# Kernel tuning notes

Hardware: AMD Instinct MI355X
Metric: run time of the kernel (lower is better)

The kernel has to match this reference:

```python
import jax, jax.numpy as jnp
import numpy as np

T, H = 2048, 2048            # tokens, hidden_size
NQ, NKV, D = 32, 4, 128      # q heads, kv heads, head_dim
E, K, I, CAP = 64, 8, 768, 512  # experts, top_k, moe_intermediate, per-expert capacity
EPS, THETA = 1e-6, 10000.0


def setup_inputs() -> dict:
    key = jax.random.key(0)
    ks = jax.random.split(key, 10)
    n = lambda k, shp, sc: jax.random.normal(k, shp, jnp.float32) * sc
    return {
        "hidden_states": n(ks[0], (T, H), 1.0),
        "positions": jnp.arange(T, dtype=jnp.int32),
        "wqkv": n(ks[1], (H, (NQ + 2 * NKV) * D), H ** -0.5),
        "wo": n(ks[2], (NQ * D, H), (NQ * D) ** -0.5),
        "q_norm_w": jnp.ones((D,), jnp.float32),
        "k_norm_w": jnp.ones((D,), jnp.float32),
        "ln1_w": jnp.ones((H,), jnp.float32),
        "ln2_w": jnp.ones((H,), jnp.float32),
        "gate_w": n(ks[3], (H, E), H ** -0.5),
        "w_gate": n(ks[4], (E, H, I), H ** -0.5),
        "w_up": n(ks[5], (E, H, I), H ** -0.5),
        "w_down": n(ks[6], (E, I, H), I ** -0.5),
    }


def _rmsnorm(x, w):
    v = jnp.mean(jnp.square(x.astype(jnp.float32)), axis=-1, keepdims=True)
    return (x.astype(jnp.float32) * jax.lax.rsqrt(v + EPS)).astype(x.dtype) * w


def _rope(x, cos, sin):
    # x: [T, heads, D]; neox-style rotate-half over full head_dim
    x1, x2 = x[..., : D // 2], x[..., D // 2:]
    c, s = cos[:, None, :], sin[:, None, :]
    return jnp.concatenate([x1 * c - x2 * s, x2 * c + x1 * s], axis=-1)


def _forward(hidden_states, positions, wqkv, wo, q_norm_w, k_norm_w, ln1_w, ln2_w, gate_w, w_gate, w_up, w_down):
    x = hidden_states
    # ---- input RMSNorm + GQA attention with QK-norm + RoPE ----
    h = _rmsnorm(x, ln1_w)
    qkv = h @ wqkv
    q, k, v = jnp.split(qkv, [NQ * D, NQ * D + NKV * D], axis=-1)
    q = _rmsnorm(q.reshape(T, NQ, D), q_norm_w)
    k = _rmsnorm(k.reshape(T, NKV, D), k_norm_w)
    v = v.reshape(T, NKV, D)
    inv_freq = 1.0 / (THETA ** (jnp.arange(0, D, 2, dtype=jnp.float32) / D))
    ang = positions.astype(jnp.float32)[:, None] * inv_freq  # [T, D/2]
    cos, sin = jnp.cos(ang), jnp.sin(ang)
    q, k = _rope(q, cos, sin), _rope(k, cos, sin)
    rep = NQ // NKV
    kr = jnp.repeat(k, rep, axis=1)  # [T, NQ, D]
    vr = jnp.repeat(v, rep, axis=1)
    scores = jnp.einsum('qhd,khd->hqk', q, kr) * (D ** -0.5)
    causal = jnp.tril(jnp.ones((T, T), bool))
    scores = jnp.where(causal[None], scores, -1e30)
    probs = jax.nn.softmax(scores, axis=-1)
    attn = jnp.einsum('hqk,khd->qhd', probs, vr).reshape(T, NQ * D)
    x = x + attn @ wo
    # ---- post-attn RMSNorm + sparse MoE (softmax top-k routing, renormalized) ----
    h = _rmsnorm(x, ln2_w)
    logits = h @ gate_w
    gate_probs = jax.nn.softmax(logits.astype(jnp.float32), axis=-1)
    topk_w, topk_idx = jax.lax.top_k(gate_probs, K)              # [T, K]
    topk_w = topk_w / jnp.sum(topk_w, axis=-1, keepdims=True)    # norm_topk_prob
    flat_e = topk_idx.reshape(-1)                                # [T*K], row-major
    oh = jax.nn.one_hot(flat_e, E, dtype=jnp.int32)
    pos = jnp.sum(jnp.cumsum(oh, axis=0) * oh, axis=-1) - 1      # slot within expert
    x_rep = jnp.repeat(h, K, axis=0)                             # [T*K, H]
    buf = jnp.zeros((E, CAP, H), h.dtype).at[flat_e, pos].set(x_rep, mode='drop')
    g = jnp.einsum('ech,ehi->eci', buf, w_gate)
    u = jnp.einsum('ech,ehi->eci', buf, w_up)
    act = jax.nn.silu(g) * u
    out_buf = jnp.einsum('eci,eih->ech', act, w_down)
    valid = (pos < CAP).astype(h.dtype)                          # CAP >> expected load; no drops in practice
    gathered = out_buf[flat_e, jnp.clip(pos, 0, CAP - 1)]        # [T*K, H]
    w = topk_w.reshape(-1).astype(h.dtype) * valid
    moe_out = jnp.sum((gathered * w[:, None]).reshape(T, K, H), axis=1)
    return x + moe_out


def reference(hidden_states, positions, wqkv, wo, q_norm_w, k_norm_w, ln1_w, ln2_w, gate_w, w_gate, w_up, w_down):
    return _forward(hidden_states, positions, wqkv, wo, q_norm_w, k_norm_w,
                    ln1_w, ln2_w, gate_w, w_gate, w_up, w_down)
```

## Files before the change

kernel.cpp:

```cpp
#include <hip/hip_runtime.h>
#include <hip/hip_bf16.h>

#define T_    2048
#define H_    2048
#define NQ_   32
#define NKV_  4
#define D_    128
#define E_    64
#define TK_   8
#define I_    768
#define CAP_  512
#define QKVW_ 5120

typedef float  f32x4  __attribute__((ext_vector_type(4)));
typedef __bf16 bf16x8 __attribute__((ext_vector_type(8)));
typedef int    i32x4  __attribute__((ext_vector_type(4)));
#define AS1 __attribute__((address_space(1)))
#define AS3 __attribute__((address_space(3)))

static __device__ __forceinline__ unsigned f2bf_u(float f){
  unsigned u = __builtin_bit_cast(unsigned, f);
  u += 0x7fffu + ((u >> 16) & 1u);
  return u >> 16;
}
static __device__ __forceinline__ float bf2f(unsigned h){
  unsigned u = h << 16;
  return __builtin_bit_cast(float, u);
}
struct HL { int h; int l; };
static __device__ __forceinline__ HL packsplit(float a, float b){
  unsigned ah = f2bf_u(a), bh = f2bf_u(b);
  float al = a - bf2f(ah), bl = b - bf2f(bh);
  HL r;
  r.h = (int)(ah | (bh << 16));
  r.l = (int)(f2bf_u(al) | (f2bf_u(bl) << 16));
  return r;
}
static __device__ __forceinline__ f32x4 mfma16(bf16x8 a, bf16x8 b, f32x4 c){
  return __builtin_amdgcn_mfma_f32_16x16x32_bf16(a, b, c, 0, 0, 0);
}

__global__ __launch_bounds__(256) void k_rms(const float* __restrict__ in,
                                             const float* __restrict__ w,
                                             unsigned short* __restrict__ outh,
                                             unsigned short* __restrict__ outl,
                                             float* __restrict__ cpy)
{
  const int t = blockIdx.x, tid = threadIdx.x;
  const float* row = in + (long)t * H_;
  float4 a = *(const float4*)(row + tid*8);
  float4 b = *(const float4*)(row + tid*8 + 4);
  float ss = a.x*a.x + a.y*a.y + a.z*a.z + a.w*a.w
           + b.x*b.x + b.y*b.y + b.z*b.z + b.w*b.w;
  #pragma unroll
  for (int o = 32; o >= 1; o >>= 1) ss += __shfl_xor(ss, o);
  __shared__ float red[4];
  if ((tid & 63) == 0) red[tid >> 6] = ss;
  __syncthreads();
  float tot = red[0] + red[1] + red[2] + red[3];
  float rs = rsqrtf(tot * (1.0f / (float)H_) + 1e-6f);
  const float* wp = w + tid*8;
  float vv[8] = {a.x, a.y, a.z, a.w, b.x, b.y, b.z, b.w};
  i32x4 oh, ol;
  #pragma unroll
  for (int d = 0; d < 4; d++){
    float v0 = vv[2*d]   * rs * wp[2*d];
    float v1 = vv[2*d+1] * rs * wp[2*d+1];
    HL r = packsplit(v0, v1);
    oh[d] = r.h; ol[d] = r.l;
  }
  *(i32x4*)(outh + (long)t * H_ + tid*8) = oh;
  if (outl) *(i32x4*)(outl + (long)t * H_ + tid*8) = ol;
  if (cpy){
    *(float4*)(cpy + (long)t * H_ + tid*8)     = a;
    *(float4*)(cpy + (long)t * H_ + tid*8 + 4) = b;
  }
}

__global__ __launch_bounds__(64) void k_ropetab(const int* __restrict__ pos,
                                                float* __restrict__ cosb,
                                                float* __restrict__ sinb)
{
  int t = blockIdx.x, j = threadIdx.x;
  float p = (float)pos[t];
  float freq = expf(-(float)j * (2.0f / (float)D_) * 9.210340371976184f);
  float ang = p * freq;
  cosb[t*64 + j] = cosf(ang);
  sinb[t*64 + j] = sinf(ang);
}

__global__ __launch_bounds__(256) void k_qknorm(const float* __restrict__ qkv,
                                                const float* __restrict__ qw,
                                                const float* __restrict__ kw,
                                                const float* __restrict__ cosb,
                                                const float* __restrict__ sinb,
                                                unsigned short* __restrict__ qh,
                                                unsigned short* __restrict__ ql,
                                                unsigned short* __restrict__ khp,
                                                unsigned short* __restrict__ klp)
{
  int gw = blockIdx.x*4 + (threadIdx.x >> 6);
  int lane = threadIdx.x & 63;
  int t = gw / 36, hh = gw - t*36;
  const float* src; const float* w;
  unsigned short *dh, *dl;
  if (hh < NQ_){
    src = qkv + (long)t*QKVW_ + hh*D_;
    w = qw;
    dh = qh + ((long)t*NQ_ + hh)*D_;
    dl = ql + ((long)t*NQ_ + hh)*D_;
  } else {
    int kh = hh - NQ_;
    src = qkv + (long)t*QKVW_ + NQ_*D_ + kh*D_;
    w = kw;
    dh = khp + ((long)t*NKV_ + kh)*D_;
    dl = klp + ((long)t*NKV_ + kh)*D_;
  }
  float a = src[lane], b = src[lane + 64];
  float ss = a*a + b*b;
  #pragma unroll
  for (int o = 32; o >= 1; o >>= 1) ss += __shfl_xor(ss, o);
  float rs = rsqrtf(ss * (1.0f / (float)D_) + 1e-6f);
  a *= rs * w[lane];
  b *= rs * w[lane + 64];
  float c = cosb[t*64 + lane], s = sinb[t*64 + lane];
  float r0 = a*c - b*s;
  float r1 = b*c + a*s;
  unsigned h0 = f2bf_u(r0), h1 = f2bf_u(r1);
  dh[lane]      = (unsigned short)h0;
  dh[lane + 64] = (unsigned short)h1;
  dl[lane]      = (unsigned short)f2bf_u(r0 - bf2f(h0));
  dl[lane + 64] = (unsigned short)f2bf_u(r1 - bf2f(h1));
}

__global__ __launch_bounds__(256) void k_vtrans(const float* __restrict__ qkv,
                                                unsigned short* __restrict__ vth,
                                                unsigned short* __restrict__ vtl)
{
  __shared__ unsigned short tileh[64][136];
  __shared__ unsigned short tilel[64][136];
  const int t0 = blockIdx.x * 64;
  const int hv = blockIdx.y;
  const int tid = threadIdx.x;
  #pragma unroll
  for (int it = 0; it < 8; it++){
    int chunk = tid + it*256;
    int r  = chunk >> 5;
    int c4 = chunk & 31;
    float4 v = *(const float4*)(qkv + (long)(t0 + r)*QKVW_ + (NQ_+NKV_)*D_ + hv*D_ + c4*4);
    float vals[4] = {v.x, v.y, v.z, v.w};
    #pragma unroll
    for (int q = 0; q < 4; q++){
      unsigned hi = f2bf_u(vals[q]);
      tileh[r][c4*4+q] = (unsigned short)hi;
      tilel[r][c4*4+q] = (unsigned short)f2bf_u(vals[q] - bf2f(hi));
    }
  }
  __syncthreads();
  int d = tid >> 1, hf = tid & 1;
  long dbase = ((long)(hv*D_ + d))*T_ + t0 + hf*32;
  #pragma unroll
  for (int k = 0; k < 4; k++){
    i32x4 oh, ol;
    #pragma unroll
    for (int d2 = 0; d2 < 4; d2++){
      int r0 = hf*32 + k*8 + d2*2, r1 = r0 + 1;
      oh[d2] = (int)((unsigned)tileh[r0][d] | ((unsigned)tileh[r1][d] << 16));
      ol[d2] = (int)((unsigned)tilel[r0][d] | ((unsigned)tilel[r1][d] << 16));
    }
    *(i32x4*)(vth + dbase + k*8) = oh;
    *(i32x4*)(vtl + dbase + k*8) = ol;
  }
}

#define VISSUE(G, BUF) { \
  const int kst_ = (G) >> 2, dp_ = (G) & 3; \
  _Pragma("unroll") \
  for (int dd = 0; dd < 2; dd++){ \
    int dn_ = dp_*2 + dd; \
    long voff = ((long)(hk*D_ + dn_*16 + l15))*T_ + kv0 + kst_*32 + g16*8; \
    BUF[dd*2]   = *(const bf16x8*)(vth + voff); \
    BUF[dd*2+1] = *(const bf16x8*)(vtl + voff); \
  } }
#define VPV(G, BUF) { \
  const int kst_ = (G) >> 2, dp_ = (G) & 3; \
  _Pragma("unroll") \
  for (int dd = 0; dd < 2; dd++){ \
    int dn_ = dp_*2 + dd; \
    o[dn_] = mfma16(pah[kst_], BUF[dd*2+1], o[dn_]); \
    o[dn_] = mfma16(pal[kst_], BUF[dd*2],   o[dn_]); \
    o[dn_] = mfma16(pah[kst_], BUF[dd*2],   o[dn_]); \
  } }

__global__ __launch_bounds__(256,2) void k_attn(const unsigned short* __restrict__ qbh,
                                                const unsigned short* __restrict__ qbl,
                                                const unsigned short* __restrict__ kbh,
                                                const unsigned short* __restrict__ kbl,
                                                const unsigned short* __restrict__ vth,
                                                const unsigned short* __restrict__ vtl,
                                                unsigned short* __restrict__ abh,
                                                unsigned short* __restrict__ abl)
{
  __shared__ char ldsK[2][2][16384];
  const int b   = blockIdx.x;
  const int xcd = b & 7, kk = xcd >> 1;
  const int s_  = ((b >> 3) << 1) | (xcd & 1);
  const int h   = kk*8 + (s_ >> 4);
  const int p   = s_ & 15;
  const int hk  = kk;
  const int tid = threadIdx.x;
  const int wv  = tid >> 6, lane = tid & 63;
  const int l15 = lane & 15, g16 = lane >> 4;
  const float sc = 0.08838834764831845f;

  long gb[4];
  #pragma unroll
  for (int i = 0; i < 4; i++){
    int srow = i*16 + (tid >> 4);
    int c = (tid & 15) ^ (srow & 7);
    gb[i] = ((long)srow*NKV_ + hk)*D_ + c*8;
  }

  for (int ph = 0; ph < 2; ph++){
    const int qt  = ph ? p : (31 - p);
    const int q0  = qt*64 + wv*16;
    const int ntB = qt + 1;

    bf16x8 qfh[4], qfl[4];
    {
      long qoff = ((long)(q0 + l15)*NQ_ + h)*D_ + g16*8;
      #pragma unroll
      for (int ks = 0; ks < 4; ks++){
        qfh[ks] = *(const bf16x8*)(qbh + qoff + ks*32);
        qfl[ks] = *(const bf16x8*)(qbl + qoff + ks*32);
      }
    }

    f32x4 zz = {0.f,0.f,0.f,0.f};
    f32x4 o[8];
    #pragma unroll
    for (int dn = 0; dn < 8; dn++) o[dn] = zz;
    float m_run = -1e30f, l_run = 0.f;

    __syncthreads();
    #pragma unroll
    for (int i = 0; i < 4; i++){
      __builtin_amdgcn_global_load_lds((const AS1 int*)(kbh + gb[i]),
          (AS3 int*)((AS3 char*)&ldsK[0][0][0] + i*4096 + tid*16), 16, 0, 0);
      __builtin_amdgcn_global_load_lds((const AS1 int*)(kbl + gb[i]),
          (AS3 int*)((AS3 char*)&ldsK[0][1][0] + i*4096 + tid*16), 16, 0, 0);
    }

    for (int t = 0; t < ntB; t++){
      __syncthreads();
      const int kv0 = t*64;
      if (t+1 < ntB){
        long kadd = (long)(t+1)*64*NKV_*D_;
        int nb = (t+1) & 1;
        #pragma unroll
        for (int i = 0; i < 4; i++){
          __builtin_amdgcn_global_load_lds((const AS1 int*)(kbh + gb[i] + kadd),
              (AS3 int*)((AS3 char*)&ldsK[nb][0][0] + i*4096 + tid*16), 16, 0, 0);
          __builtin_amdgcn_global_load_lds((const AS1 int*)(kbl + gb[i] + kadd),
              (AS3 int*)((AS3 char*)&ldsK[nb][1][0] + i*4096 + tid*16), 16, 0, 0);
        }
      }
      {
        const char* Kh = &ldsK[t & 1][0][0];
        const char* Kl = &ldsK[t & 1][1][0];
        f32x4 sA[4];
        #pragma unroll
        for (int sub = 0; sub < 4; sub++) sA[sub] = zz;
        __builtin_amdgcn_s_setprio(1);
        #pragma unroll
        for (int sub = 0; sub < 4; sub++){
          int row = sub*16 + l15;
          int rsw = (row & 7) << 4;
          #pragma unroll
          for (int ks = 0; ks < 4; ks++){
            bf16x8 kh = *(const bf16x8*)(Kh + row*256 + (((ks*4 + g16)*16) ^ rsw));
            bf16x8 kl = *(const bf16x8*)(Kl + row*256 + (((ks*4 + g16)*16) ^ rsw));
            sA[sub] = mfma16(kh, qfl[ks], sA[sub]);
            sA[sub] = mfma16(kl, qfh[ks], sA[sub]);
            sA[sub] = mfma16(kh, qfh[ks], sA[sub]);
          }
        }
        __builtin_amdgcn_s_setprio(0);
        bf16x8 vA[4], vB[4];
        VISSUE(0, vA);
        {
          int qrow = q0 + l15;
          float mt = -1e30f;
          #pragma unroll
          for (int sub = 0; sub < 4; sub++)
            #pragma unroll
            for (int r = 0; r < 4; r++){
              int kva = kv0 + sub*16 + g16*4 + r;
              float v = sA[sub][r]*sc;
              if (kva > qrow) v = -1e30f;
              sA[sub][r] = v;
              mt = fmaxf(mt, v);
            }
          mt = fmaxf(mt, __shfl_xor(mt,16));
          mt = fmaxf(mt, __shfl_xor(mt,32));
          float mnew = fmaxf(m_run, mt);
          float corr = __expf(m_run - mnew);
          float ps = 0.f;
          #pragma unroll
          for (int sub = 0; sub < 4; sub++)
            #pragma unroll
            for (int r = 0; r < 4; r++){
              float e = __expf(sA[sub][r] - mnew);
              sA[sub][r] = e;
              ps += e;
            }
          ps += __shfl_xor(ps,16);
          ps += __shfl_xor(ps,32);
          l_run = l_run*corr + ps;
          m_run = mnew;
          #pragma unroll
          for (int r = 0; r < 4; r++){
            float cr = __shfl(corr, g16*4 + r);
            #pragma unroll
            for (int dn = 0; dn < 8; dn++) o[dn][r] *= cr;
          }
        }
        bf16x8 pah[2], pal[2];
        #pragma unroll
        for (int kst = 0; kst < 2; kst++){
          f32x4 s0 = sA[2*kst], s1 = sA[2*kst+1];
          i32x4 pkh, pkl;
          #pragma unroll
          for (int d = 0; d < 4; d++){
            const int e0 = 2*d, e1 = 2*d+1;
            int src0 = (((2*g16 + (e0>>2)) & 3) << 4) | l15;
            int src1 = (((2*g16 + (e1>>2)) & 3) << 4) | l15;
            float a0t = __shfl(s0[e0&3], src0), a1t = __shfl(s1[e0&3], src0);
            float b0t = __shfl(s0[e1&3], src1), b1t = __shfl(s1[e1&3], src1);
            float va = (g16 >= 2) ? a1t : a0t;
            float vb = (g16 >= 2) ? b1t : b0t;
            HL r = packsplit(va, vb);
            pkh[d] = r.h; pkl[d] = r.l;
          }
          pah[kst] = __builtin_bit_cast(bf16x8, pkh);
          pal[kst] = __builtin_bit_cast(bf16x8, pkl);
        }
        VISSUE(1, vB);
        __builtin_amdgcn_s_setprio(1);
        VPV(0, vA); VISSUE(2, vA);
        VPV(1, vB); VISSUE(3, vB);
        VPV(2, vA); VISSUE(4, vA);
        VPV(3, vB); VISSUE(5, vB);
        VPV(4, vA); VISSUE(6, vA);
        VPV(5, vB); VISSUE(7, vB);
        VPV(6, vA);
        VPV(7, vB);
        __builtin_amdgcn_s_setprio(0);
      }
    }

    {
      float linv = 1.0f / l_run;
      #pragma unroll
      for (int r = 0; r < 4; r++){
        float lr = __shfl(linv, g16*4 + r);
        long row = q0 + g16*4 + r;
        #pragma unroll
        for (int dn = 0; dn < 8; dn++){
          float v = o[dn][r]*lr;
          unsigned hi = f2bf_u(v);
          long idx = row*(NQ_*D_) + h*D_ + dn*16 + l15;
          abh[idx] = (unsigned short)hi;
          abl[idx] = (unsigned short)f2bf_u(v - bf2f(hi));
        }
      }
    }
  }
}

struct SA {
  const unsigned short* Ah;
  const unsigned short* Al;
  const float* B;
  int lda, ldb, K, ldc;
  float* Cf;
  const float* add;
};

template<int MODE>
__global__ __launch_bounds__(256,2) void k_gs(SA ga)
{
  __shared__ unsigned short ldsAh[128*64];
  __shared__ unsigned short ldsAl[128*64];
  __shared__ unsigned short ldsBh[8*128*8];
  __shared__ unsigned short ldsBl[8*128*8];
  const int tid = threadIdx.x;
  const int lane = tid & 63;
  const int wv = tid >> 6;
  const int wm = (wv >> 1)*64, wn = (wv & 1)*64;
  const int l15 = lane & 15, g16 = lane >> 4;

  const long m0 = (long)blockIdx.y * 128;
  const long n0 = (long)blockIdx.x * 128;

  long aoff[4];
  #pragma unroll
  for (int i = 0; i < 4; i++){
    int chunk = tid + i*256;
    int m = chunk >> 3, c = chunk & 7;
    aoff[i] = (m0 + m) * (long)ga.lda + c*8;
  }
  const float* brow = ga.B + n0 + (long)((tid >> 5)*8) * ga.ldb + (tid & 31)*4;

  f32x4 zz = {0.f,0.f,0.f,0.f};
  f32x4 acc[4][4];
  #pragma unroll
  for (int i = 0; i < 4; i++)
    #pragma unroll
    for (int j = 0; j < 4; j++) acc[i][j] = zz;

  i32x4 pva[4], pvl[4];
  float4 pb[8];
  #pragma unroll
  for (int i = 0; i < 4; i++){
    pva[i] = *(const i32x4*)(ga.Ah + aoff[i]);
    pvl[i] = *(const i32x4*)(ga.Al + aoff[i]);
  }
  #pragma unroll
  for (int r = 0; r < 8; r++) pb[r] = *(const float4*)(brow + (long)r * ga.ldb);

  for (int kt = 0; kt < ga.K; kt += 64){
    __syncthreads();
    #pragma unroll
    for (int i = 0; i < 4; i++){
      int chunk = tid + i*256;
      int m = chunk >> 3, c = chunk & 7;
      int sw = (c*16) ^ ((m & 7) << 4);
      *(i32x4*)((char*)ldsAh + m*128 + sw) = pva[i];
      *(i32x4*)((char*)ldsAl + m*128 + sw) = pvl[i];
    }
    {
      i32x4 ph0, ph1, ph2, ph3, pl0, pl1, pl2, pl3;
      #pragma unroll
      for (int r = 0; r < 8; r += 2){
        float4 va = pb[r];
        float4 vb = pb[r+1];
        int d = r >> 1;
        HL rx = packsplit(va.x, vb.x); ph0[d] = rx.h; pl0[d] = rx.l;
        HL ry = packsplit(va.y, vb.y); ph1[d] = ry.h; pl1[d] = ry.l;
        HL rz = packsplit(va.z, vb.z); ph2[d] = rz.h; pl2[d] = rz.l;
        HL rw = packsplit(va.w, vb.w); ph3[d] = rw.h; pl3[d] = rw.l;
      }
      int kbb = tid >> 5, nb = (tid & 31)*4;
      long bo = ((long)kbb*128 + nb) << 4;
      char* bph = (char*)ldsBh + bo;
      char* bpl = (char*)ldsBl + bo;
      *(i32x4*)(bph)      = ph0;  *(i32x4*)(bpl)      = pl0;
      *(i32x4*)(bph + 16) = ph1;  *(i32x4*)(bpl + 16) = pl1;
      *(i32x4*)(bph + 32) = ph2;  *(i32x4*)(bpl + 32) = pl2;
      *(i32x4*)(bph + 48) = ph3;  *(i32x4*)(bpl + 48) = pl3;
    }
    __syncthreads();
    if (kt + 64 < ga.K){
      #pragma unroll
      for (int i = 0; i < 4; i++){
        pva[i] = *(const i32x4*)(ga.Ah + aoff[i] + kt + 64);
        pvl[i] = *(const i32x4*)(ga.Al + aoff[i] + kt + 64);
      }
      #pragma unroll
      for (int r = 0; r < 8; r++) pb[r] = *(const float4*)(brow + (long)(kt + 64 + r) * ga.ldb);
    }
    #pragma unroll
    for (int ks = 0; ks < 2; ks++){
      bf16x8 afh[4], afl[4], bfh[4], bfl[4];
      #pragma unroll
      for (int i = 0; i < 4; i++){
        int m = wm + i*16 + l15;
        int sw = (ks*64 + g16*16) ^ ((m & 7) << 4);
        afh[i] = *(const bf16x8*)((const char*)ldsAh + m*128 + sw);
        afl[i] = *(const bf16x8*)((const char*)ldsAl + m*128 + sw);
      }
      #pragma unroll
      for (int j = 0; j < 4; j++){
        int n = wn + j*16 + l15;
        long bo = ((long)(ks*4 + g16)*128 + n) << 4;
        bfh[j] = *(const bf16x8*)((const char*)ldsBh + bo);
        bfl[j] = *(const bf16x8*)((const char*)ldsBl + bo);
      }
      #pragma unroll
      for (int i = 0; i < 4; i++)
        #pragma unroll
        for (int j = 0; j < 4; j++){
          acc[i][j] = mfma16(afh[i], bfl[j], acc[i][j]);
          acc[i][j] = mfma16(afl[i], bfh[j], acc[i][j]);
          acc[i][j] = mfma16(afh[i], bfh[j], acc[i][j]);
        }
    }
  }

  #pragma unroll
  for (int i = 0; i < 4; i++){
    #pragma unroll
    for (int j = 0; j < 4; j++){
      #pragma unroll
      for (int r = 0; r < 4; r++){
        float v = acc[i][j][r];
        long grow = m0 + wm + i*16 + g16*4 + r;
        long gcol = n0 + wn + j*16 + l15;
        long idx = grow * ga.ldc + gcol;
        if (MODE == 0) ga.Cf[idx] = v;
        else           ga.Cf[idx] = v + ga.add[idx];
      }
    }
  }
}

__global__ __launch_bounds__(256,2) void k_logits(const unsigned short* __restrict__ Ah,
                                                  const unsigned short* __restrict__ Al,
                                                  const float* __restrict__ B,
                                                  float* __restrict__ logits)
{
  __shared__ unsigned short ldsAh[256*64];
  __shared__ unsigned short ldsAl[256*64];
  __shared__ unsigned short ldsBh[8*64*8];
  __shared__ unsigned short ldsBl[8*64*8];
  const int tid = threadIdx.x, lane = tid & 63, wv = tid >> 6;
  const int l15 = lane & 15, g16 = lane >> 4;
  const long m0 = (long)blockIdx.x * 256;

  long aoff[8];
  #pragma unroll
  for (int i = 0; i < 8; i++){
    int chunk = tid + i*256;
    int m = chunk >> 3, c = chunk & 7;
    int csw = c ^ (m & 7);
    aoff[i] = (m0 + m) * (long)H_ + csw*8;
  }
  const float* brow = B + (long)((tid >> 5)*8) * E_ + (tid & 31)*2;

  f32x4 zz = {0.f,0.f,0.f,0.f};
  f32x4 acc[4][4];
  #pragma unroll
  for (int i = 0; i < 4; i++)
    #pragma unroll
    for (int j = 0; j < 4; j++) acc[i][j] = zz;

  float2 pb[8];
  #pragma unroll
  for (int r = 0; r < 8; r++) pb[r] = *(const float2*)(brow + (long)r * E_);

  for (int kt = 0; kt < H_; kt += 64){
    __syncthreads();
    #pragma unroll
    for (int i = 0; i < 8; i++){
      __builtin_amdgcn_global_load_lds((const AS1 int*)(Ah + aoff[i] + kt),
          (AS3 int*)((AS3 char*)ldsAh + i*4096 + tid*16), 16, 0, 0);
      __builtin_amdgcn_global_load_lds((const AS1 int*)(Al + aoff[i] + kt),
          (AS3 int*)((AS3 char*)ldsAl + i*4096 + tid*16), 16, 0, 0);
    }
    {
      i32x4 p0h, p0l, p1h, p1l;
      #pragma unroll
      for (int r = 0; r < 8; r += 2){
        int d = r >> 1;
        HL rx = packsplit(pb[r].x, pb[r+1].x); p0h[d] = rx.h; p0l[d] = rx.l;
        HL ry = packsplit(pb[r].y, pb[r+1].y); p1h[d] = ry.h; p1l[d] = ry.l;
      }
      int kbb = tid >> 5, nb = (tid & 31)*2;
      long bo = ((long)kbb*64 + nb) << 4;
      *(i32x4*)((char*)ldsBh + bo)      = p0h;
      *(i32x4*)((char*)ldsBh + bo + 16) = p1h;
      *(i32x4*)((char*)ldsBl + bo)      = p0l;
      *(i32x4*)((char*)ldsBl + bo + 16) = p1l;
    }
    __syncthreads();
    if (kt + 64 < H_){
      #pragma unroll
      for (int r = 0; r < 8; r++) pb[r] = *(const float2*)(brow + (long)(kt + 64 + r) * E_);
    }
    #pragma unroll
    for (int ks = 0; ks < 2; ks++){
      bf16x8 afh[4], afl[4], bfh[4], bfl[4];
      #pragma unroll
      for (int i = 0; i < 4; i++){
        int m = wv*64 + i*16 + l15;
        int sw = (ks*64 + g16*16) ^ ((m & 7) << 4);
        afh[i] = *(const bf16x8*)((const char*)ldsAh + m*128 + sw);
        afl[i] = *(const bf16x8*)((const char*)ldsAl + m*128 + sw);
      }
      #pragma unroll
      for (int j = 0; j < 4; j++){
        int n = j*16 + l15;
        long bo = ((long)(ks*4 + g16)*64 + n) << 4;
        bfh[j] = *(const bf16x8*)((const char*)ldsBh + bo);
        bfl[j] = *(const bf16x8*)((const char*)ldsBl + bo);
      }
      #pragma unroll
      for (int i = 0; i < 4; i++)
        #pragma unroll
        for (int j = 0; j < 4; j++){
          acc[i][j] = mfma16(afh[i], bfl[j], acc[i][j]);
          acc[i][j] = mfma16(afl[i], bfh[j], acc[i][j]);
          acc[i][j] = mfma16(afh[i], bfh[j], acc[i][j]);
        }
    }
  }

  #pragma unroll
  for (int i = 0; i < 4; i++)
    #pragma unroll
    for (int j = 0; j < 4; j++)
      #pragma unroll
      for (int r = 0; r < 4; r++){
        long row = m0 + wv*64 + i*16 + g16*4 + r;
        logits[row*E_ + j*16 + l15] = acc[i][j][r];
      }
}

__global__ __launch_bounds__(64) void k_router2(const float* __restrict__ logits,
                                                int* __restrict__ tidx,
                                                float* __restrict__ twv)
{
  __shared__ int   ti[8];
  __shared__ float tv[8];
  const int t = blockIdx.x, lane = threadIdx.x;
  float acc = logits[(long)t*E_ + lane];
  float mx = acc;
  #pragma unroll
  for (int o = 32; o >= 1; o >>= 1) mx = fmaxf(mx, __shfl_xor(mx, o));
  float p = __expf(acc - mx);
  float sm = p;
  #pragma unroll
  for (int o = 32; o >= 1; o >>= 1) sm += __shfl_xor(sm, o);
  p /= sm;
  float cur = p, wsum = 0.f;
  #pragma unroll
  for (int j = 0; j < 8; j++){
    float v = cur; int ix = lane;
    #pragma unroll
    for (int o = 1; o < 64; o <<= 1){
      float ov = __shfl_xor(v, o); int oi = __shfl_xor(ix, o);
      if (ov > v || (ov == v && oi < ix)){ v = ov; ix = oi; }
    }
    if (lane == ix) cur = -1.f;
    wsum += v;
    if (lane == 0){ ti[j] = ix; tv[j] = v; }
  }
  __syncthreads();
  if (lane < 8){
    tidx[t*TK_ + lane] = ti[lane];
    twv [t*TK_ + lane] = tv[lane] / wsum;
  }
}

struct GA {
  const unsigned short* A;
  const float* B;
  const float* B2;
  int lda, ldb, K, ldc;
  unsigned short* Cb;
  const int* rowidx;
  const float* wslot;
  const int* counts;
  float* outp;
};

template<int MODE>
__global__ __launch_bounds__(256,3) void k_gemm(GA ga)
{
  __shared__ unsigned short ldsA[256*64];
  __shared__ unsigned short ldsB[8*64*8];
  const int tid = threadIdx.x;
  const int lane = tid & 63;
  const int wv = tid >> 6;
  const int l15 = lane & 15, g16 = lane >> 4;

  long m0 = (long)blockIdx.y * 256;
  long n0 = 0;
  const unsigned short* A = ga.A;
  const int* rowmap = nullptr;
  int e = blockIdx.z, count = ga.counts[e];
  if ((int)m0 >= count) return;

  const float* bbase;
  {
    int c2 = (tid & 31) * 2;
    if (MODE == 2){
      n0 = (long)blockIdx.x * 32;
      rowmap = ga.rowidx + e * CAP_;
      if (c2 < 32) bbase = ga.B  + (long)e * H_ * I_ + n0 + c2;
      else         bbase = ga.B2 + (long)e * H_ * I_ + n0 + (c2 - 32);
    } else {
      n0 = (long)blockIdx.x * 64;
      bbase = ga.B + (long)e * I_ * H_ + n0 + c2;
      A = ga.A + (long)e * CAP_ * I_;
    }
  }

  const unsigned short* arow[8];
  #pragma unroll
  for (int i = 0; i < 8; i++){
    int chunk = tid + i*256;
    int m = chunk >> 3, c = chunk & 7;
    int csw = c ^ (m & 7);
    int s = (int)m0 + m; if (s > count - 1) s = count - 1;
    long row = (MODE == 2) ? (long)rowmap[s] : (long)s;
    arow[i] = A + row * (long)ga.lda + csw*8;
  }
  const float* brow = bbase + (long)((tid >> 5)*8) * ga.ldb;

  f32x4 zz = {0.f,0.f,0.f,0.f};
  f32x4 acc[4][4];
  #pragma unroll
  for (int i = 0; i < 4; i++)
    #pragma unroll
    for (int j = 0; j < 4; j++) acc[i][j] = zz;

  float2 pb[8];
  #pragma unroll
  for (int r = 0; r < 8; r++) pb[r] = *(const float2*)(brow + (long)r * ga.ldb);

  for (int kt = 0; kt < ga.K; kt += 64){
    __syncthreads();
    #pragma unroll
    for (int i = 0; i < 8; i++){
      __builtin_amdgcn_global_load_lds((const AS1 int*)(arow[i] + kt),
          (AS3 int*)((AS3 char*)ldsA + i*4096 + tid*16), 16, 0, 0);
    }
    {
      i32x4 p0, p1;
      #pragma unroll
      for (int r = 0; r < 8; r += 2){
        int d = r >> 1;
        p0[d] = (int)(f2bf_u(pb[r].x) | (f2bf_u(pb[r+1].x) << 16));
        p1[d] = (int)(f2bf_u(pb[r].y) | (f2bf_u(pb[r+1].y) << 16));
      }
      int kbb = tid >> 5, nb = (tid & 31)*2;
      char* bp = (char*)ldsB + (((long)kbb*64 + nb) << 4);
      *(i32x4*)(bp)      = p0;
      *(i32x4*)(bp + 16) = p1;
    }
    __syncthreads();
    if (kt + 64 < ga.K){
      #pragma unroll
      for (int r = 0; r < 8; r++) pb[r] = *(const float2*)(brow + (long)(kt + 64 + r) * ga.ldb);
    }
    #pragma unroll
    for (int ks = 0; ks < 2; ks++){
      bf16x8 af[4], bfv[4];
      #pragma unroll
      for (int i = 0; i < 4; i++){
        int m = wv*64 + i*16 + l15;
        af[i] = *(const bf16x8*)((const char*)ldsA + m*128 + ((ks*64 + g16*16) ^ ((m & 7) << 4)));
      }
      #pragma unroll
      for (int j = 0; j < 4; j++){
        int n = j*16 + l15;
        bfv[j] = *(const bf16x8*)((const char*)ldsB + (((long)(ks*4 + g16)*64 + n) << 4));
      }
      #pragma unroll
      for (int i = 0; i < 4; i++)
        #pragma unroll
        for (int j = 0; j < 4; j++)
          acc[i][j] = mfma16(af[i], bfv[j], acc[i][j]);
    }
  }

  if (MODE == 2){
    #pragma unroll
    for (int i = 0; i < 4; i++){
      #pragma unroll
      for (int jj = 0; jj < 2; jj++){
        #pragma unroll
        for (int r = 0; r < 4; r++){
          float g = acc[i][jj][r];
          float u = acc[i][jj+2][r];
          float actv = g / (1.f + __expf(-g)) * u;
          int grow = (int)m0 + wv*64 + i*16 + g16*4 + r;
          if (grow < count)
            ga.Cb[((long)e*CAP_ + grow)*I_ + n0 + jj*16 + l15] = (unsigned short)f2bf_u(actv);
        }
      }
    }
  } else {
    #pragma unroll
    for (int i = 0; i < 4; i++){
      #pragma unroll
      for (int j = 0; j < 4; j++){
        #pragma unroll
        for (int r = 0; r < 4; r++){
          float v = acc[i][j][r];
          int grow = (int)m0 + wv*64 + i*16 + g16*4 + r;
          long gcol = n0 + j*16 + l15;
          if (grow < count){
            float ww = ga.wslot[e*CAP_ + grow];
            int tk = ga.rowidx[e*CAP_ + grow];
            atomicAdd(ga.outp + (long)tk*H_ + gcol, v*ww);
          }
        }
      }
    }
  }
}

__global__ __launch_bounds__(64) void k_route(const int* __restrict__ tidx,
                                              const float* __restrict__ twv,
                                              int* __restrict__ rowi,
                                              float* __restrict__ wsl,
                                              int* __restrict__ cnts)
{
  const int e = blockIdx.x, lane = threadIdx.x;
  int run = 0;
  for (int s0 = 0; s0 < T_*TK_; s0 += 64){
    int s = s0 + lane;
    int idx = tidx[s];
    bool m = (idx == e);
    unsigned long long mk = __ballot(m);
    int pre = __popcll(mk & ((1ull << lane) - 1ull));
    int pos = run + pre;
    if (m && pos < CAP_){
      rowi[e*CAP_ + pos] = s >> 3;
      wsl [e*CAP_ + pos] = twv[s];
    }
    run += __popcll(mk);
  }
  if (lane == 0) cnts[e] = (run < CAP_) ? run : CAP_;
}

extern "C" void kernel_launch(void* const* d_in, const int* in_sizes, int n_in,
                              void* d_out, int out_size, void* d_ws, size_t ws_size,
                              hipStream_t stream)
{
  (void)in_sizes; (void)n_in; (void)out_size; (void)ws_size;
  const float* x    = (const float*)d_in[0];
  const int*   pos  = (const int*)d_in[1];
  const float* wqkv = (const float*)d_in[2];
  const float* wo   = (const float*)d_in[3];
  const float* qnw  = (const float*)d_in[4];
  const float* knw  = (const float*)d_in[5];
  const float* ln1  = (const float*)d_in[6];
  const float* ln2  = (const float*)d_in[7];
  const float* gwt  = (const float*)d_in[8];
  const float* wg   = (const float*)d_in[9];
  const float* wu   = (const float*)d_in[10];
  const float* wd   = (const float*)d_in[11];
  float* out = (float*)d_out;

  char* ws = (char*)d_ws;
  size_t off = 0;
  auto alloc = [&](size_t b)->void*{ void* p = ws + off; off += (b + 255) & ~(size_t)255; return p; };

  unsigned short* hbh = (unsigned short*)alloc((size_t)T_*H_*2);
  unsigned short* hbl = (unsigned short*)alloc((size_t)T_*H_*2);
  float* qkv          = (float*)alloc((size_t)T_*QKVW_*4);
  float* cosb         = (float*)alloc((size_t)T_*64*4);
  float* sinb         = (float*)alloc((size_t)T_*64*4);
  unsigned short* qbh = (unsigned short*)alloc((size_t)T_*NQ_*D_*2);
  unsigned short* qbl = (unsigned short*)alloc((size_t)T_*NQ_*D_*2);
  unsigned short* kbh = (unsigned short*)alloc((size_t)T_*NKV_*D_*2);
  unsigned short* kbl = (unsigned short*)alloc((size_t)T_*NKV_*D_*2);
  unsigned short* vth = (unsigned short*)alloc((size_t)NKV_*D_*T_*2);
  unsigned short* vtl = (unsigned short*)alloc((size_t)NKV_*D_*T_*2);
  unsigned short* abh = (unsigned short*)alloc((size_t)T_*NQ_*D_*2);
  unsigned short* abl = (unsigned short*)alloc((size_t)T_*NQ_*D_*2);
  float* x2           = (float*)alloc((size_t)T_*H_*4);
  unsigned short* h2b = (unsigned short*)alloc((size_t)T_*H_*2);
  unsigned short* h2l = (unsigned short*)alloc((size_t)T_*H_*2);
  float* lgt          = (float*)alloc((size_t)T_*E_*4);
  int* tidx           = (int*)alloc((size_t)T_*TK_*4);
  float* twv          = (float*)alloc((size_t)T_*TK_*4);
  int* rowi           = (int*)alloc((size_t)E_*CAP_*4);
  float* wsl          = (float*)alloc((size_t)E_*CAP_*4);
  int* cnts           = (int*)alloc((size_t)E_*4);
  unsigned short* gu  = (unsigned short*)alloc((size_t)E_*CAP_*I_*2);

  k_rms<<<T_, 256, 0, stream>>>(x, ln1, hbh, hbl, nullptr);
  k_ropetab<<<T_, 64, 0, stream>>>(pos, cosb, sinb);
  {
    SA a{}; a.Ah = hbh; a.Al = hbl; a.B = wqkv; a.lda = H_; a.ldb = QKVW_; a.K = H_; a.ldc = QKVW_; a.Cf = qkv;
    k_gs<0><<<dim3(QKVW_/128, T_/128), 256, 0, stream>>>(a);
  }
  k_qknorm<<<T_*36/4, 256, 0, stream>>>(qkv, qnw, knw, cosb, sinb, qbh, qbl, kbh, kbl);
  k_vtrans<<<dim3(T_/64, NKV_), 256, 0, stream>>>(qkv, vth, vtl);
  k_attn<<<512, 256, 0, stream>>>(qbh, qbl, kbh, kbl, vth, vtl, abh, abl);
  {
    SA a{}; a.Ah = abh; a.Al = abl; a.B = wo; a.lda = NQ_*D_; a.ldb = H_; a.K = NQ_*D_; a.ldc = H_;
    a.Cf = x2; a.add = x;
    k_gs<1><<<dim3(H_/128, T_/128), 256, 0, stream>>>(a);
  }
  k_rms<<<T_, 256, 0, stream>>>(x2, ln2, h2b, h2l, out);
  k_logits<<<T_/256, 256, 0, stream>>>(h2b, h2l, gwt, lgt);
  k_router2<<<T_, 64, 0, stream>>>(lgt, tidx, twv);
  k_route<<<E_, 64, 0, stream>>>(tidx, twv, rowi, wsl, cnts);
  {
    GA a{}; a.A = h2b; a.B = wg; a.B2 = wu; a.lda = H_; a.ldb = I_; a.K = H_;
    a.Cb = gu; a.rowidx = rowi; a.counts = cnts;
    k_gemm<2><<<dim3(24, 2, E_), 256, 0, stream>>>(a);
  }
  {
    GA a{}; a.A = gu; a.B = wd; a.lda = I_; a.ldb = H_; a.K = I_;
    a.counts = cnts; a.rowidx = rowi; a.wslot = wsl; a.outp = out;
    k_gemm<3><<<dim3(32, 2, E_), 256, 0, stream>>>(a);
  }
}
```

Before: 1.439 ms.

## Double-buffer MoE GEMM LDS tiles with K-step 32 and single barrier

Restructures the expert GEMM main loop to use two LDS buffers with a K tile of 32 instead of a single buffer with K tile of 64. The next tile's A loads (direct global-to-LDS) and converted B writes are issued before computing the current tile, so one barrier per iteration replaces two. B loading changes from float2 pairs to scalar per-column loads. This trades a halved K step, meaning more iterations and more loop and barrier overhead, and narrower B loads for overlap of memory traffic with MFMA work. The total LDS footprint is unchanged.

```diff
diff --git a/kernel.cpp b/kernel.cpp
--- a/kernel.cpp
+++ b/kernel.cpp
@@ -668,8 +668,8 @@
 template<int MODE>
 __global__ __launch_bounds__(256,3) void k_gemm(GA ga)
 {
-  __shared__ unsigned short ldsA[256*64];
-  __shared__ unsigned short ldsB[8*64*8];
+  __shared__ unsigned short ldsA[2][256*32];
+  __shared__ unsigned short ldsB[2][4*64*8];
   const int tid = threadIdx.x;
   const int lane = tid & 63;
   const int wv = tid >> 6;
@@ -682,32 +682,29 @@
   int e = blockIdx.z, count = ga.counts[e];
   if ((int)m0 >= count) return;
 
-  const float* bbase;
-  {
-    int c2 = (tid & 31) * 2;
-    if (MODE == 2){
-      n0 = (long)blockIdx.x * 32;
-      rowmap = ga.rowidx + e * CAP_;
-      if (c2 < 32) bbase = ga.B  + (long)e * H_ * I_ + n0 + c2;
-      else         bbase = ga.B2 + (long)e * H_ * I_ + n0 + (c2 - 32);
-    } else {
-      n0 = (long)blockIdx.x * 64;
-      bbase = ga.B + (long)e * I_ * H_ + n0 + c2;
-      A = ga.A + (long)e * CAP_ * I_;
-    }
-  }
-
-  const unsigned short* arow[8];
-  #pragma unroll
-  for (int i = 0; i < 8; i++){
+  const int kb = tid >> 6, nb = tid & 63;
+  const float* bcol;
+  if (MODE == 2){
+    n0 = (long)blockIdx.x * 32;
+    rowmap = ga.rowidx + e * CAP_;
+    if (nb < 32) bcol = ga.B  + (long)e * H_ * I_ + n0 + nb;
+    else         bcol = ga.B2 + (long)e * H_ * I_ + n0 + (nb - 32);
+  } else {
+    n0 = (long)blockIdx.x * 64;
+    bcol = ga.B + (long)e * I_ * H_ + n0 + nb;
+    A = ga.A + (long)e * CAP_ * I_;
+  }
+
+  const unsigned short* arow[4];
+  #pragma unroll
+  for (int i = 0; i < 4; i++){
     int chunk = tid + i*256;
-    int m = chunk >> 3, c = chunk & 7;
-    int csw = c ^ (m & 7);
+    int m = chunk >> 2, c = chunk & 3;
+    int csw = c ^ (m & 3);
     int s = (int)m0 + m; if (s > count - 1) s = count - 1;
     long row = (MODE == 2) ? (long)rowmap[s] : (long)s;
     arow[i] = A + row * (long)ga.lda + csw*8;
   }
-  const float* brow = bbase + (long)((tid >> 5)*8) * ga.ldb;
 
   f32x4 zz = {0.f,0.f,0.f,0.f};
   f32x4 acc[4][4];
@@ -716,47 +713,62 @@
     #pragma unroll
     for (int j = 0; j < 4; j++) acc[i][j] = zz;
 
-  float2 pb[8];
-  #pragma unroll
-  for (int r = 0; r < 8; r++) pb[r] = *(const float2*)(brow + (long)r * ga.ldb);
-
-  for (int kt = 0; kt < ga.K; kt += 64){
+  const int nt = ga.K / 32;
+  float pbv[8];
+
+  #pragma unroll
+  for (int i = 0; i < 4; i++){
+    __builtin_amdgcn_global_load_lds((const AS1 int*)(arow[i]),
+        (AS3 int*)((AS3 char*)&ldsA[0][0] + i*4096 + tid*16), 16, 0, 0);
+  }
+  #pragma unroll
+  for (int j = 0; j < 8; j++) pbv[j] = bcol[(long)(kb*8 + j) * ga.ldb];
+  {
+    i32x4 p0;
+    #pragma unroll
+    for (int d = 0; d < 4; d++)
+      p0[d] = (int)(f2bf_u(pbv[2*d]) | (f2bf_u(pbv[2*d+1]) << 16));
+    *(i32x4*)((char*)&ldsB[0][0] + ((kb*64 + nb) << 4)) = p0;
+  }
+  if (nt > 1){
+    #pragma unroll
+    for (int j = 0; j < 8; j++) pbv[j] = bcol[(long)(32 + kb*8 + j) * ga.ldb];
+  }
+
+  for (int t = 0; t < nt; t++){
     __syncthreads();
-    #pragma unroll
-    for (int i = 0; i < 8; i++){
-      __builtin_amdgcn_global_load_lds((const AS1 int*)(arow[i] + kt),
-          (AS3 int*)((AS3 char*)ldsA + i*4096 + tid*16), 16, 0, 0);
+    if (t+1 < nt){
+      const int nbuf = (t+1) & 1;
+      const int ktn = (t+1) * 32;
+      #pragma unroll
+      for (int i = 0; i < 4; i++){
+        __builtin_amdgcn_global_load_lds((const AS1 int*)(arow[i] + ktn),
+            (AS3 int*)((AS3 char*)&ldsA[nbuf][0] + i*4096 + tid*16), 16, 0, 0);
+      }
+      i32x4 p0;
+      #pragma unroll
+      for (int d = 0; d < 4; d++)
+        p0[d] = (int)(f2bf_u(pbv[2*d]) | (f2bf_u(pbv[2*d+1]) << 16));
+      *(i32x4*)((char*)&ldsB[nbuf][0] + ((kb*64 + nb) << 4)) = p0;
+      if (t+2 < nt){
+        const int ktn2 = (t+2) * 32;
+        #pragma unroll
+        for (int j = 0; j < 8; j++) pbv[j] = bcol[(long)(ktn2 + kb*8 + j) * ga.ldb];
+      }
     }
     {
-      i32x4 p0, p1;
-      #pragma unroll
-      for (int r = 0; r < 8; r += 2){
-        int d = r >> 1;
-        p0[d] = (int)(f2bf_u(pb[r].x) | (f2bf_u(pb[r+1].x) << 16));
-        p1[d] = (int)(f2bf_u(pb[r].y) | (f2bf_u(pb[r+1].y) << 16));
-      }
-      int kbb = tid >> 5, nb = (tid & 31)*2;
-      char* bp = (char*)ldsB + (((long)kbb*64 + nb) << 4);
-      *(i32x4*)(bp)      = p0;
-      *(i32x4*)(bp + 16) = p1;
-    }
-    __syncthreads();
-    if (kt + 64 < ga.K){
-      #pragma unroll
-      for (int r = 0; r < 8; r++) pb[r] = *(const float2*)(brow + (long)(kt + 64 + r) * ga.ldb);
-    }
-    #pragma unroll
-    for (int ks = 0; ks < 2; ks++){
+      const char* La = (const char*)&ldsA[t & 1][0];
+      const char* Lb = (const char*)&ldsB[t & 1][0];
       bf16x8 af[4], bfv[4];
       #pragma unroll
       for (int i = 0; i < 4; i++){
         int m = wv*64 + i*16 + l15;
-        af[i] = *(const bf16x8*)((const char*)ldsA + m*128 + ((ks*64 + g16*16) ^ ((m & 7) << 4)));
+        af[i] = *(const bf16x8*)(La + m*64 + ((g16*16) ^ ((m & 3) << 4)));
       }
       #pragma unroll
       for (int j = 0; j < 4; j++){
         int n = j*16 + l15;
-        bfv[j] = *(const bf16x8*)((const char*)ldsB + (((long)(ks*4 + g16)*64 + n) << 4));
+        bfv[j] = *(const bf16x8*)(Lb + ((g16*64 + n) << 4));
       }
       #pragma unroll
       for (int i = 0; i < 4; i++)
```

Measured after the change: 1.509 ms. 4.9% more time.

## Double-buffer LDS tiles in MoE GEMM with manual waitcnt pipelining

Applied to the files above, without the earlier changes.

Splits the A and B shared-memory tiles into two buffers so the global-to-LDS loads for the next K tile are issued while MFMAs run on the current tile. The B loads are prefetched two tiles ahead, and explicit s_waitcnt vmcnt values with scheduling barriers control when data must be resident. Occupancy drops from 3 to 2 blocks per CU because LDS use doubles. The hand-counted vmcnt thresholds are fragile and could allow a race if the compiler emits a different number of loads.

```diff
diff --git a/kernel.cpp b/kernel.cpp
--- a/kernel.cpp
+++ b/kernel.cpp
@@ -666,10 +666,10 @@
 };
 
 template<int MODE>
-__global__ __launch_bounds__(256,3) void k_gemm(GA ga)
-{
-  __shared__ unsigned short ldsA[256*64];
-  __shared__ unsigned short ldsB[8*64*8];
+__global__ __launch_bounds__(256,2) void k_gemm(GA ga)
+{
+  __shared__ unsigned short ldsA[2][256*64];
+  __shared__ unsigned short ldsB[2][8*64*8];
   const int tid = threadIdx.x;
   const int lane = tid & 63;
   const int wv = tid >> 6;
@@ -716,55 +716,82 @@
     #pragma unroll
     for (int j = 0; j < 4; j++) acc[i][j] = zz;
 
+  const int nt = ga.K / 64;
   float2 pb[8];
-  #pragma unroll
-  for (int r = 0; r < 8; r++) pb[r] = *(const float2*)(brow + (long)r * ga.ldb);
-
-  for (int kt = 0; kt < ga.K; kt += 64){
-    __syncthreads();
-    #pragma unroll
-    for (int i = 0; i < 8; i++){
-      __builtin_amdgcn_global_load_lds((const AS1 int*)(arow[i] + kt),
-          (AS3 int*)((AS3 char*)ldsA + i*4096 + tid*16), 16, 0, 0);
-    }
+
+  #define AISSUE(TT) { \
+    unsigned short* adst_ = &ldsA[(TT) & 1][0]; \
+    _Pragma("unroll") \
+    for (int i = 0; i < 8; i++) \
+      __builtin_amdgcn_global_load_lds((const AS1 int*)(arow[i] + (TT)*64), \
+          (AS3 int*)((AS3 char*)adst_ + i*4096 + tid*16), 16, 0, 0); \
+  }
+  #define BLOAD(TT) { \
+    _Pragma("unroll") \
+    for (int r = 0; r < 8; r++) \
+      pb[r] = *(const float2*)(brow + (long)((TT)*64 + r) * ga.ldb); \
+  }
+  #define BWRITE(TT) { \
+    i32x4 p0_, p1_; \
+    _Pragma("unroll") \
+    for (int r = 0; r < 8; r += 2){ \
+      int d = r >> 1; \
+      p0_[d] = (int)(f2bf_u(pb[r].x) | (f2bf_u(pb[r+1].x) << 16)); \
+      p1_[d] = (int)(f2bf_u(pb[r].y) | (f2bf_u(pb[r+1].y) << 16)); \
+    } \
+    int kbb_ = tid >> 5, nb2_ = (tid & 31)*2; \
+    char* bp_ = (char*)&ldsB[(TT) & 1][0] + (((long)kbb_*64 + nb2_) << 4); \
+    *(i32x4*)(bp_)      = p0_; \
+    *(i32x4*)(bp_ + 16) = p1_; \
+  }
+
+  AISSUE(0);
+  BLOAD(0);
+  BWRITE(0);
+  if (nt > 1) BLOAD(1);
+
+  for (int t = 0; t < nt; t++){
+    __builtin_amdgcn_sched_barrier(0);
+    __builtin_amdgcn_s_barrier();
+    __builtin_amdgcn_sched_barrier(0);
+    if (t+1 < nt){
+      AISSUE(t+1);
+      BWRITE(t+1);
+      if (t+2 < nt) BLOAD(t+2);
+    }
+    __builtin_amdgcn_sched_barrier(0);
+    if (t+2 < nt)      asm volatile("s_waitcnt vmcnt(16) lgkmcnt(0)" ::: "memory");
+    else if (t+1 < nt) asm volatile("s_waitcnt vmcnt(8) lgkmcnt(0)" ::: "memory");
+    else               asm volatile("s_waitcnt vmcnt(0) lgkmcnt(0)" ::: "memory");
+    __builtin_amdgcn_s_barrier();
+    __builtin_amdgcn_sched_barrier(0);
     {
-      i32x4 p0, p1;
-      #pragma unroll
-      for (int r = 0; r < 8; r += 2){
-        int d = r >> 1;
-        p0[d] = (int)(f2bf_u(pb[r].x) | (f2bf_u(pb[r+1].x) << 16));
-        p1[d] = (int)(f2bf_u(pb[r].y) | (f2bf_u(pb[r+1].y) << 16));
-      }
-      int kbb = tid >> 5, nb = (tid & 31)*2;
-      char* bp = (char*)ldsB + (((long)kbb*64 + nb) << 4);
-      *(i32x4*)(bp)      = p0;
-      *(i32x4*)(bp + 16) = p1;
-    }
-    __syncthreads();
-    if (kt + 64 < ga.K){
-      #pragma unroll
-      for (int r = 0; r < 8; r++) pb[r] = *(const float2*)(brow + (long)(kt + 64 + r) * ga.ldb);
-    }
-    #pragma unroll
-    for (int ks = 0; ks < 2; ks++){
-      bf16x8 af[4], bfv[4];
-      #pragma unroll
-      for (int i = 0; i < 4; i++){
-        int m = wv*64 + i*16 + l15;
-        af[i] = *(const bf16x8*)((const char*)ldsA + m*128 + ((ks*64 + g16*16) ^ ((m & 7) << 4)));
-      }
-      #pragma unroll
-      for (int j = 0; j < 4; j++){
-        int n = j*16 + l15;
-        bfv[j] = *(const bf16x8*)((const char*)ldsB + (((long)(ks*4 + g16)*64 + n) << 4));
-      }
-      #pragma unroll
-      for (int i = 0; i < 4; i++)
-        #pragma unroll
-        for (int j = 0; j < 4; j++)
-          acc[i][j] = mfma16(af[i], bfv[j], acc[i][j]);
-    }
-  }
+      const char* La = (const char*)&ldsA[t & 1][0];
+      const char* Lb = (const char*)&ldsB[t & 1][0];
+      #pragma unroll
+      for (int ks = 0; ks < 2; ks++){
+        bf16x8 af[4], bfv[4];
+        #pragma unroll
+        for (int i = 0; i < 4; i++){
+          int m = wv*64 + i*16 + l15;
+          af[i] = *(const bf16x8*)(La + m*128 + ((ks*64 + g16*16) ^ ((m & 7) << 4)));
+        }
+        #pragma unroll
+        for (int j = 0; j < 4; j++){
+          int n = j*16 + l15;
+          bfv[j] = *(const bf16x8*)(Lb + (((long)(ks*4 + g16)*64 + n) << 4));
+        }
+        #pragma unroll
+        for (int i = 0; i < 4; i++)
+          #pragma unroll
+          for (int j = 0; j < 4; j++)
+            acc[i][j] = mfma16(af[i], bfv[j], acc[i][j]);
+      }
+    }
+  }
+  #undef AISSUE
+  #undef BLOAD
+  #undef BWRITE
 
   if (MODE == 2){
     #pragma unroll
```

Measured after the change: 1.599 ms. 1.11x slower.
